# Kernel tuning notes

Hardware: AMD Instinct MI355X
Metric: run time of the kernel (lower is better)

## Reference

```python
import jax, jax.numpy as jnp
import numpy as np

N_NODES = 100000
N_EDGES = 1600000
IN_DIM, HIDDEN, OUT = 256, 128, 64


def setup_inputs() -> dict:
    key = jax.random.key(0)
    k1, k2, k3, k4 = jax.random.split(key, 4)
    x = jax.random.normal(k1, (N_NODES, IN_DIM), dtype=jnp.float32)
    edge_index = jax.random.randint(k2, (2, N_EDGES), 0, N_NODES, dtype=jnp.int32)
    # glorot-ish init for the GCN linear layers
    W1 = jax.random.normal(k3, (IN_DIM, HIDDEN), dtype=jnp.float32) / np.sqrt(IN_DIM)
    b1 = jnp.zeros((HIDDEN,), dtype=jnp.float32)
    W2 = jax.random.normal(k4, (HIDDEN, OUT), dtype=jnp.float32) / np.sqrt(HIDDEN)
    b2 = jnp.zeros((OUT,), dtype=jnp.float32)
    return {"x": x, "edge_index": edge_index, "W1": W1, "b1": b1, "W2": W2, "b2": b2}


def gcn_layer(x, src, dst, W, b):
    """PyG GCNConv: add self-loops, symmetric deg^-1/2 normalization,
    linear transform, scatter-add aggregation, bias."""
    h = x @ W  # [N, F_out]
    # degree over self-looped graph: in-degree(dst counts) + 1 self loop
    deg = jax.ops.segment_sum(jnp.ones((src.shape[0],), h.dtype), dst,
                              num_segments=N_NODES) + 1.0
    dinv = jax.lax.rsqrt(deg)  # [N]
    coef = dinv[src] * dinv[dst]  # [E]
    agg = jax.ops.segment_sum(h[src] * coef[:, None], dst, num_segments=N_NODES)
    # self-loop contribution (norm = dinv[i]^2) without materializing loop edges
    agg = agg + h * (dinv * dinv)[:, None]
    return agg + b


def reference(x, edge_index, W1, b1, W2, b2):
    src, dst = edge_index[0], edge_index[1]
    h = jax.nn.relu(gcn_layer(x, src, dst, W1, b1))
    return jax.nn.relu(gcn_layer(h, src, dst, W2, b2))
```

## Files before the change

kernel.cpp:

```cpp
#include <hip/hip_runtime.h>

#define N_NODES 100000
#define N_EDGES 1600000
#define IN_DIM 256
#define HIDDEN 128
#define OUT_DIM 64
#define LDA 40

#define NBIN 391
#define NBLK3 256
#define CHUNK 6250
#define NMAT (NBIN * NBLK3)
#define NBLK_SCAN (NMAT / 256)
#define CAP 6144

typedef __bf16 bf16x8 __attribute__((ext_vector_type(8)));
typedef __bf16 bf16x4 __attribute__((ext_vector_type(4)));
typedef float f32x4 __attribute__((ext_vector_type(4)));

__launch_bounds__(256)
__global__ void k_hist(const int* __restrict__ dst, int* __restrict__ cnt2) {
    __shared__ int hist[NBIN];
    for (int i = threadIdx.x; i < NBIN; i += 256) hist[i] = 0;
    __syncthreads();
    int base = blockIdx.x * CHUNK;
    for (int i = threadIdx.x; i < CHUNK; i += 256)
        atomicAdd(&hist[dst[base + i] >> 8], 1);
    __syncthreads();
    for (int k = threadIdx.x; k < NBIN; k += 256)
        cnt2[k * NBLK3 + blockIdx.x] = hist[k];
}

__global__ void k_scan1(int* __restrict__ a, int* __restrict__ bsum) {
    __shared__ int tmp[256];
    int t = threadIdx.x;
    int i = blockIdx.x * 256 + t;
    int v = a[i];
    tmp[t] = v;
    __syncthreads();
    #pragma unroll
    for (int off = 1; off < 256; off <<= 1) {
        int p = (t >= off) ? tmp[t - off] : 0;
        __syncthreads();
        tmp[t] += p;
        __syncthreads();
    }
    a[i] = tmp[t] - v;
    if (t == 255) bsum[blockIdx.x] = tmp[255];
}

__global__ void k_scan2(int* __restrict__ bsum) {
    __shared__ int tmp[512];
    int t = threadIdx.x;
    int v = (t < NBLK_SCAN) ? bsum[t] : 0;
    tmp[t] = v;
    __syncthreads();
    #pragma unroll
    for (int off = 1; off < 512; off <<= 1) {
        int p = (t >= off) ? tmp[t - off] : 0;
        __syncthreads();
        tmp[t] += p;
        __syncthreads();
    }
    if (t < NBLK_SCAN) bsum[t] = tmp[t] - v;
}

__global__ void k_scan3(int* __restrict__ a, const int* __restrict__ bsum) {
    int i = blockIdx.x * 256 + threadIdx.x;
    a[i] += bsum[blockIdx.x];
}

__launch_bounds__(256)
__global__ void k_scatter_bins(const int* __restrict__ src, const int* __restrict__ dst,
                               const int* __restrict__ off2,
                               unsigned int* __restrict__ ebuf) {
    __shared__ int cursor[NBIN];
    for (int k = threadIdx.x; k < NBIN; k += 256)
        cursor[k] = off2[k * NBLK3 + blockIdx.x];
    __syncthreads();
    int base = blockIdx.x * CHUNK;
    for (int i = threadIdx.x; i < CHUNK; i += 256) {
        int s = src[base + i], d = dst[base + i];
        int pos = atomicAdd(&cursor[d >> 8], 1);
        ebuf[pos] = ((unsigned)s << 8) | (unsigned)(d & 255);
    }
}

__launch_bounds__(256)
__global__ void k_fine(const unsigned int* __restrict__ ebuf, const int* __restrict__ off2,
                       int* __restrict__ esrc, int* __restrict__ rowstart,
                       float* __restrict__ dinv) {
    __shared__ int hist[256];
    __shared__ int tmp[256];
    __shared__ int nodeoff[256];
    __shared__ int cursor[256];
    __shared__ unsigned int ed[CAP];
    __shared__ int sOut[CAP];

    const int k = blockIdx.x;
    const int t = threadIdx.x;
    const int e0 = off2[k * NBLK3];
    const int e1 = (k + 1 < NBIN) ? off2[(k + 1) * NBLK3] : N_EDGES;
    int m = e1 - e0;
    if (m > CAP) m = CAP;

    hist[t] = 0;
    __syncthreads();
    for (int i = t; i < m; i += 256) {
        unsigned v = ebuf[e0 + i];
        ed[i] = v;
        atomicAdd(&hist[v & 255], 1);
    }
    __syncthreads();

    int v = hist[t];
    tmp[t] = v;
    __syncthreads();
    #pragma unroll
    for (int off = 1; off < 256; off <<= 1) {
        int p = (t >= off) ? tmp[t - off] : 0;
        __syncthreads();
        tmp[t] += p;
        __syncthreads();
    }
    nodeoff[t] = tmp[t] - v;
    cursor[t] = tmp[t] - v;
    __syncthreads();

    for (int i = t; i < m; i += 256) {
        unsigned e = ed[i];
        int pos = atomicAdd(&cursor[e & 255], 1);
        sOut[pos] = (int)(e >> 8);
    }
    __syncthreads();

    for (int i = t; i < m; i += 256) esrc[e0 + i] = sOut[i];

    int n = k * 256 + t;
    if (n < N_NODES) {
        rowstart[n] = e0 + nodeoff[t];
        dinv[n] = rsqrtf((float)hist[t] + 1.0f);
    }
    if (k == 0 && t == 0) rowstart[N_NODES] = N_EDGES;
}

__launch_bounds__(256, 2)
__global__ void k_gemm1(const float* __restrict__ X, const float* __restrict__ W1,
                        __bf16* __restrict__ H) {
    __shared__ __attribute__((aligned(16))) __bf16 As[128 * LDA];
    __shared__ __attribute__((aligned(16))) __bf16 Bs[128 * LDA];

    const int t = threadIdx.x;
    const int wave = t >> 6;
    const int lane = t & 63;
    const int wr = wave >> 1, wc = wave & 1;
    const int lm = lane & 15;
    const int q = lane >> 4;
    const int row0 = blockIdx.x * 128;

    f32x4 acc[4][4] = {};

    for (int k0 = 0; k0 < IN_DIM; k0 += 32) {
        #pragma unroll
        for (int p = 0; p < 4; ++p) {
            int r = p * 32 + (t >> 3);
            int kk = (t & 7) * 4;
            int g = row0 + r;
            float4 v = make_float4(0.f, 0.f, 0.f, 0.f);
            if (g < N_NODES) v = *(const float4*)&X[g * IN_DIM + k0 + kk];
            __bf16* dp = &As[r * LDA + kk];
            dp[0] = (__bf16)v.x; dp[1] = (__bf16)v.y;
            dp[2] = (__bf16)v.z; dp[3] = (__bf16)v.w;
        }
        #pragma unroll
        for (int p = 0; p < 4; ++p) {
            int idx = p * 256 + t;
            int kk = idx >> 5;
            int c = (idx & 31) * 4;
            float4 v = *(const float4*)&W1[(k0 + kk) * HIDDEN + c];
            Bs[(c + 0) * LDA + kk] = (__bf16)v.x;
            Bs[(c + 1) * LDA + kk] = (__bf16)v.y;
            Bs[(c + 2) * LDA + kk] = (__bf16)v.z;
            Bs[(c + 3) * LDA + kk] = (__bf16)v.w;
        }
        __syncthreads();

        bf16x8 af[4], bfr[4];
        #pragma unroll
        for (int mi = 0; mi < 4; ++mi)
            af[mi] = *(const bf16x8*)&As[(wr * 64 + mi * 16 + lm) * LDA + q * 8];
        #pragma unroll
        for (int ni = 0; ni < 4; ++ni)
            bfr[ni] = *(const bf16x8*)&Bs[(wc * 64 + ni * 16 + lm) * LDA + q * 8];
        #pragma unroll
        for (int mi = 0; mi < 4; ++mi)
            #pragma unroll
            for (int ni = 0; ni < 4; ++ni)
                acc[mi][ni] = __builtin_amdgcn_mfma_f32_16x16x32_bf16(
                    af[mi], bfr[ni], acc[mi][ni], 0, 0, 0);
        __syncthreads();
    }

    #pragma unroll
    for (int mi = 0; mi < 4; ++mi) {
        #pragma unroll
        for (int r = 0; r < 4; ++r) {
            int grow = row0 + wr * 64 + mi * 16 + q * 4 + r;
            if (grow < N_NODES) {
                #pragma unroll
                for (int ni = 0; ni < 4; ++ni) {
                    int col = wc * 64 + ni * 16 + lm;
                    H[grow * HIDDEN + col] = (__bf16)acc[mi][ni][r];
                }
            }
        }
    }
}

__launch_bounds__(256)
__global__ void k_gather1(const int* __restrict__ rowstart, const int* __restrict__ esrc,
                          const float* __restrict__ dinv,
                          const __bf16* __restrict__ H, const float* __restrict__ b1,
                          __bf16* __restrict__ AGG) {
    int n = blockIdx.x * 16 + (threadIdx.x >> 4);
    if (n >= N_NODES) return;
    int j = (threadIdx.x & 15) * 8;

    float dn = dinv[n];
    float s = dn * dn;
    bf16x8 h = *(const bf16x8*)&H[n * HIDDEN + j];
    float acc[8];
    #pragma unroll
    for (int i = 0; i < 8; ++i) acc[i] = (float)h[i] * s;

    int p0 = rowstart[n], p1 = rowstart[n + 1];
    int p = p0;
    for (; p + 3 < p1; p += 4) {
        int s0 = esrc[p + 0], s1 = esrc[p + 1], s2 = esrc[p + 2], s3 = esrc[p + 3];
        float c0 = dinv[s0] * dn, c1 = dinv[s1] * dn;
        float c2 = dinv[s2] * dn, c3 = dinv[s3] * dn;
        bf16x8 v0 = *(const bf16x8*)&H[s0 * HIDDEN + j];
        bf16x8 v1 = *(const bf16x8*)&H[s1 * HIDDEN + j];
        bf16x8 v2 = *(const bf16x8*)&H[s2 * HIDDEN + j];
        bf16x8 v3 = *(const bf16x8*)&H[s3 * HIDDEN + j];
        #pragma unroll
        for (int i = 0; i < 8; ++i) acc[i] = fmaf((float)v0[i], c0, acc[i]);
        #pragma unroll
        for (int i = 0; i < 8; ++i) acc[i] = fmaf((float)v1[i], c1, acc[i]);
        #pragma unroll
        for (int i = 0; i < 8; ++i) acc[i] = fmaf((float)v2[i], c2, acc[i]);
        #pragma unroll
        for (int i = 0; i < 8; ++i) acc[i] = fmaf((float)v3[i], c3, acc[i]);
    }
    for (; p < p1; ++p) {
        int sidx = esrc[p];
        float c = dinv[sidx] * dn;
        bf16x8 v = *(const bf16x8*)&H[sidx * HIDDEN + j];
        #pragma unroll
        for (int i = 0; i < 8; ++i) acc[i] = fmaf((float)v[i], c, acc[i]);
    }

    float4 bb0 = *(const float4*)&b1[j];
    float4 bb1 = *(const float4*)&b1[j + 4];
    bf16x8 o;
    o[0] = (__bf16)fmaxf(acc[0] + bb0.x, 0.f);
    o[1] = (__bf16)fmaxf(acc[1] + bb0.y, 0.f);
    o[2] = (__bf16)fmaxf(acc[2] + bb0.z, 0.f);
    o[3] = (__bf16)fmaxf(acc[3] + bb0.w, 0.f);
    o[4] = (__bf16)fmaxf(acc[4] + bb1.x, 0.f);
    o[5] = (__bf16)fmaxf(acc[5] + bb1.y, 0.f);
    o[6] = (__bf16)fmaxf(acc[6] + bb1.z, 0.f);
    o[7] = (__bf16)fmaxf(acc[7] + bb1.w, 0.f);
    *(bf16x8*)&AGG[n * HIDDEN + j] = o;
}

__launch_bounds__(256, 2)
__global__ void k_gemm2(const __bf16* __restrict__ AGG, const float* __restrict__ W2,
                        __bf16* __restrict__ H2) {
    __shared__ __attribute__((aligned(16))) __bf16 As[128 * LDA];
    __shared__ __attribute__((aligned(16))) __bf16 Bs[64 * LDA];

    const int t = threadIdx.x;
    const int wave = t >> 6;
    const int lane = t & 63;
    const int lm = lane & 15;
    const int q = lane >> 4;
    const int row0 = blockIdx.x * 128;

    f32x4 acc[2][4] = {};

    for (int k0 = 0; k0 < HIDDEN; k0 += 32) {
        #pragma unroll
        for (int p = 0; p < 2; ++p) {
            int idx = p * 256 + t;
            int r = idx >> 2;
            int seg = (idx & 3) * 8;
            int g = row0 + r;
            uint4 v = make_uint4(0u, 0u, 0u, 0u);
            if (g < N_NODES) v = *(const uint4*)&AGG[g * HIDDEN + k0 + seg];
            *(uint4*)&As[r * LDA + seg] = v;
        }
        #pragma unroll
        for (int p = 0; p < 2; ++p) {
            int idx = p * 256 + t;
            int kk = idx >> 4;
            int c = (idx & 15) * 4;
            float4 v = *(const float4*)&W2[(k0 + kk) * OUT_DIM + c];
            Bs[(c + 0) * LDA + kk] = (__bf16)v.x;
            Bs[(c + 1) * LDA + kk] = (__bf16)v.y;
            Bs[(c + 2) * LDA + kk] = (__bf16)v.z;
            Bs[(c + 3) * LDA + kk] = (__bf16)v.w;
        }
        __syncthreads();

        bf16x8 af[2], bfr[4];
        #pragma unroll
        for (int mi = 0; mi < 2; ++mi)
            af[mi] = *(const bf16x8*)&As[(wave * 32 + mi * 16 + lm) * LDA + q * 8];
        #pragma unroll
        for (int ni = 0; ni < 4; ++ni)
            bfr[ni] = *(const bf16x8*)&Bs[(ni * 16 + lm) * LDA + q * 8];
        #pragma unroll
        for (int mi = 0; mi < 2; ++mi)
            #pragma unroll
            for (int ni = 0; ni < 4; ++ni)
                acc[mi][ni] = __builtin_amdgcn_mfma_f32_16x16x32_bf16(
                    af[mi], bfr[ni], acc[mi][ni], 0, 0, 0);
        __syncthreads();
    }

    #pragma unroll
    for (int mi = 0; mi < 2; ++mi) {
        #pragma unroll
        for (int r = 0; r < 4; ++r) {
            int grow = row0 + wave * 32 + mi * 16 + q * 4 + r;
            if (grow < N_NODES) {
                #pragma unroll
                for (int ni = 0; ni < 4; ++ni) {
                    int col = ni * 16 + lm;
                    H2[grow * OUT_DIM + col] = (__bf16)acc[mi][ni][r];
                }
            }
        }
    }
}

__launch_bounds__(256)
__global__ void k_gather2(const int* __restrict__ rowstart, const int* __restrict__ esrc,
                          const float* __restrict__ dinv,
                          const __bf16* __restrict__ H2, const float* __restrict__ b2,
                          float* __restrict__ OUT) {
    int n = blockIdx.x * 32 + (threadIdx.x >> 3);
    if (n >= N_NODES) return;
    int j = (threadIdx.x & 7) * 8;

    float dn = dinv[n];
    float s = dn * dn;
    bf16x8 h = *(const bf16x8*)&H2[n * OUT_DIM + j];
    float acc[8];
    #pragma unroll
    for (int i = 0; i < 8; ++i) acc[i] = (float)h[i] * s;

    int p0 = rowstart[n], p1 = rowstart[n + 1];
    int p = p0;
    for (; p + 3 < p1; p += 4) {
        int s0 = esrc[p + 0], s1 = esrc[p + 1], s2 = esrc[p + 2], s3 = esrc[p + 3];
        float c0 = dinv[s0] * dn, c1 = dinv[s1] * dn;
        float c2 = dinv[s2] * dn, c3 = dinv[s3] * dn;
        bf16x8 v0 = *(const bf16x8*)&H2[s0 * OUT_DIM + j];
        bf16x8 v1 = *(const bf16x8*)&H2[s1 * OUT_DIM + j];
        bf16x8 v2 = *(const bf16x8*)&H2[s2 * OUT_DIM + j];
        bf16x8 v3 = *(const bf16x8*)&H2[s3 * OUT_DIM + j];
        #pragma unroll
        for (int i = 0; i < 8; ++i) acc[i] = fmaf((float)v0[i], c0, acc[i]);
        #pragma unroll
        for (int i = 0; i < 8; ++i) acc[i] = fmaf((float)v1[i], c1, acc[i]);
        #pragma unroll
        for (int i = 0; i < 8; ++i) acc[i] = fmaf((float)v2[i], c2, acc[i]);
        #pragma unroll
        for (int i = 0; i < 8; ++i) acc[i] = fmaf((float)v3[i], c3, acc[i]);
    }
    for (; p < p1; ++p) {
        int sidx = esrc[p];
        float c = dinv[sidx] * dn;
        bf16x8 v = *(const bf16x8*)&H2[sidx * OUT_DIM + j];
        #pragma unroll
        for (int i = 0; i < 8; ++i) acc[i] = fmaf((float)v[i], c, acc[i]);
    }

    float4 bb0 = *(const float4*)&b2[j];
    float4 bb1 = *(const float4*)&b2[j + 4];
    float4 o0, o1;
    o0.x = fmaxf(acc[0] + bb0.x, 0.f);
    o0.y = fmaxf(acc[1] + bb0.y, 0.f);
    o0.z = fmaxf(acc[2] + bb0.z, 0.f);
    o0.w = fmaxf(acc[3] + bb0.w, 0.f);
    o1.x = fmaxf(acc[4] + bb1.x, 0.f);
    o1.y = fmaxf(acc[5] + bb1.y, 0.f);
    o1.z = fmaxf(acc[6] + bb1.z, 0.f);
    o1.w = fmaxf(acc[7] + bb1.w, 0.f);
    *(float4*)&OUT[n * OUT_DIM + j] = o0;
    *(float4*)&OUT[n * OUT_DIM + j + 4] = o1;
}

extern "C" void kernel_launch(void* const* d_in, const int* in_sizes, int n_in,
                              void* d_out, int out_size, void* d_ws, size_t ws_size,
                              hipStream_t stream) {
    const float* x  = (const float*)d_in[0];
    const int* ei   = (const int*)d_in[1];
    const float* W1 = (const float*)d_in[2];
    const float* b1 = (const float*)d_in[3];
    const float* W2 = (const float*)d_in[4];
    const float* b2 = (const float*)d_in[5];
    float* out = (float*)d_out;

    const int* src = ei;
    const int* dst = ei + N_EDGES;

    char* ws = (char*)d_ws;
    int*          cnt2     = (int*)         (ws + 0x000000);
    int*          bsum     = (int*)         (ws + 0x080000);
    int*          rowstart = (int*)         (ws + 0x090000);
    float*        dinv     = (float*)       (ws + 0x100000);
    unsigned int* ebuf     = (unsigned int*)(ws + 0x180000);
    int*          esrc     = (int*)         (ws + 0x800000);
    __bf16*       h1       = (__bf16*)      (ws + 0xE80000);
    __bf16*       agg1     = (__bf16*)      (ws + 0x2880000);
    __bf16*       h2       = (__bf16*)      (ws + 0x4280000);

    k_hist<<<NBLK3, 256, 0, stream>>>(dst, cnt2);
    k_scan1<<<NBLK_SCAN, 256, 0, stream>>>(cnt2, bsum);
    k_scan2<<<1, 512, 0, stream>>>(bsum);
    k_scan3<<<NBLK_SCAN, 256, 0, stream>>>(cnt2, bsum);
    k_scatter_bins<<<NBLK3, 256, 0, stream>>>(src, dst, cnt2, ebuf);
    k_fine<<<NBIN, 256, 0, stream>>>(ebuf, cnt2, esrc, rowstart, dinv);

    k_gemm1<<<(N_NODES + 127) / 128, 256, 0, stream>>>(x, W1, h1);
    k_gather1<<<(N_NODES + 15) / 16, 256, 0, stream>>>(rowstart, esrc, dinv, h1, b1, agg1);
    k_gemm2<<<(N_NODES + 127) / 128, 256, 0, stream>>>(agg1, W2, h2);
    k_gather2<<<(N_NODES + 31) / 32, 256, 0, stream>>>(rowstart, esrc, dinv, h2, b2, out);
}
```

Before: 349.0 us.

## Load A operands directly from global into registers and stage full weight matrix in LDS

```diff
diff --git a/kernel.cpp b/kernel.cpp
--- a/kernel.cpp
+++ b/kernel.cpp
@@ -5,7 +5,6 @@
 #define IN_DIM 256
 #define HIDDEN 128
 #define OUT_DIM 64
-#define LDA 40
 
 #define NBIN 391
 #define NBLK3 256
@@ -13,6 +12,9 @@
 #define NMAT (NBIN * NBLK3)
 #define NBLK_SCAN (NMAT / 256)
 #define CAP 6144
+
+#define LDK1 264
+#define LDK2 136
 
 typedef __bf16 bf16x8 __attribute__((ext_vector_type(8)));
 typedef __bf16 bf16x4 __attribute__((ext_vector_type(4)));
@@ -147,8 +149,7 @@
 __launch_bounds__(256, 2)
 __global__ void k_gemm1(const float* __restrict__ X, const float* __restrict__ W1,
                         __bf16* __restrict__ H) {
-    __shared__ __attribute__((aligned(16))) __bf16 As[128 * LDA];
-    __shared__ __attribute__((aligned(16))) __bf16 Bs[128 * LDA];
+    __shared__ __attribute__((aligned(16))) __bf16 Bs[HIDDEN * LDK1];
 
     const int t = threadIdx.x;
     const int wave = t >> 6;
@@ -156,62 +157,71 @@
     const int wr = wave >> 1, wc = wave & 1;
     const int lm = lane & 15;
     const int q = lane >> 4;
-    const int row0 = blockIdx.x * 128;
+    const int row0 = blockIdx.x * 128 + wr * 64;
+    const int colbase = wc * 64;
+
+    #pragma unroll
+    for (int it = 0; it < 16; ++it) {
+        int idx = it * 256 + t;
+        int k2 = idx >> 5;
+        int c = (idx & 31) * 4;
+        float4 v0 = *(const float4*)&W1[(2 * k2) * HIDDEN + c];
+        float4 v1 = *(const float4*)&W1[(2 * k2 + 1) * HIDDEN + c];
+        const float lo[4] = {v0.x, v0.y, v0.z, v0.w};
+        const float hi[4] = {v1.x, v1.y, v1.z, v1.w};
+        #pragma unroll
+        for (int i = 0; i < 4; ++i) {
+            __bf16 pair[2] = {(__bf16)lo[i], (__bf16)hi[i]};
+            *(unsigned int*)&Bs[(c + i) * LDK1 + 2 * k2] = *(unsigned int*)pair;
+        }
+    }
+    __syncthreads();
+
+    const float* xp[4];
+    #pragma unroll
+    for (int mi = 0; mi < 4; ++mi) {
+        int r = row0 + mi * 16 + lm;
+        if (r > N_NODES - 1) r = N_NODES - 1;
+        xp[mi] = &X[r * IN_DIM];
+    }
 
     f32x4 acc[4][4] = {};
 
-    for (int k0 = 0; k0 < IN_DIM; k0 += 32) {
-        #pragma unroll
-        for (int p = 0; p < 4; ++p) {
-            int r = p * 32 + (t >> 3);
-            int kk = (t & 7) * 4;
-            int g = row0 + r;
-            float4 v = make_float4(0.f, 0.f, 0.f, 0.f);
-            if (g < N_NODES) v = *(const float4*)&X[g * IN_DIM + k0 + kk];
-            __bf16* dp = &As[r * LDA + kk];
-            dp[0] = (__bf16)v.x; dp[1] = (__bf16)v.y;
-            dp[2] = (__bf16)v.z; dp[3] = (__bf16)v.w;
+    #pragma unroll
+    for (int ks = 0; ks < 8; ++ks) {
+        bf16x8 af[4];
+        #pragma unroll
+        for (int mi = 0; mi < 4; ++mi) {
+            float4 a0 = *(const float4*)&xp[mi][ks * 32 + q * 8];
+            float4 a1 = *(const float4*)&xp[mi][ks * 32 + q * 8 + 4];
+            bf16x8 f;
+            f[0] = (__bf16)a0.x; f[1] = (__bf16)a0.y;
+            f[2] = (__bf16)a0.z; f[3] = (__bf16)a0.w;
+            f[4] = (__bf16)a1.x; f[5] = (__bf16)a1.y;
+            f[6] = (__bf16)a1.z; f[7] = (__bf16)a1.w;
+            af[mi] = f;
         }
-        #pragma unroll
-        for (int p = 0; p < 4; ++p) {
-            int idx = p * 256 + t;
-            int kk = idx >> 5;
-            int c = (idx & 31) * 4;
-            float4 v = *(const float4*)&W1[(k0 + kk) * HIDDEN + c];
-            Bs[(c + 0) * LDA + kk] = (__bf16)v.x;
-            Bs[(c + 1) * LDA + kk] = (__bf16)v.y;
-            Bs[(c + 2) * LDA + kk] = (__bf16)v.z;
-            Bs[(c + 3) * LDA + kk] = (__bf16)v.w;
-        }
-        __syncthreads();
-
-        bf16x8 af[4], bfr[4];
-        #pragma unroll
-        for (int mi = 0; mi < 4; ++mi)
-            af[mi] = *(const bf16x8*)&As[(wr * 64 + mi * 16 + lm) * LDA + q * 8];
+        bf16x8 bfr[4];
         #pragma unroll
         for (int ni = 0; ni < 4; ++ni)
-            bfr[ni] = *(const bf16x8*)&Bs[(wc * 64 + ni * 16 + lm) * LDA + q * 8];
+            bfr[ni] = *(const bf16x8*)&Bs[(colbase + ni * 16 + lm) * LDK1 + ks * 32 + q * 8];
         #pragma unroll
         for (int mi = 0; mi < 4; ++mi)
             #pragma unroll
             for (int ni = 0; ni < 4; ++ni)
                 acc[mi][ni] = __builtin_amdgcn_mfma_f32_16x16x32_bf16(
                     af[mi], bfr[ni], acc[mi][ni], 0, 0, 0);
-        __syncthreads();
     }
 
     #pragma unroll
     for (int mi = 0; mi < 4; ++mi) {
         #pragma unroll
         for (int r = 0; r < 4; ++r) {
-            int grow = row0 + wr * 64 + mi * 16 + q * 4 + r;
+            int grow = row0 + mi * 16 + q * 4 + r;
             if (grow < N_NODES) {
                 #pragma unroll
-                for (int ni = 0; ni < 4; ++ni) {
-                    int col = wc * 64 + ni * 16 + lm;
-                    H[grow * HIDDEN + col] = (__bf16)acc[mi][ni][r];
-                }
+                for (int ni = 0; ni < 4; ++ni)
+                    H[grow * HIDDEN + colbase + ni * 16 + lm] = (__bf16)acc[mi][ni][r];
             }
         }
     }
@@ -277,69 +287,69 @@
 __launch_bounds__(256, 2)
 __global__ void k_gemm2(const __bf16* __restrict__ AGG, const float* __restrict__ W2,
                         __bf16* __restrict__ H2) {
-    __shared__ __attribute__((aligned(16))) __bf16 As[128 * LDA];
-    __shared__ __attribute__((aligned(16))) __bf16 Bs[64 * LDA];
+    __shared__ __attribute__((aligned(16))) __bf16 Bs[OUT_DIM * LDK2];
 
     const int t = threadIdx.x;
     const int wave = t >> 6;
     const int lane = t & 63;
     const int lm = lane & 15;
     const int q = lane >> 4;
-    const int row0 = blockIdx.x * 128;
-
-    f32x4 acc[2][4] = {};
-
-    for (int k0 = 0; k0 < HIDDEN; k0 += 32) {
-        #pragma unroll
-        for (int p = 0; p < 2; ++p) {
-            int idx = p * 256 + t;
-            int r = idx >> 2;
-            int seg = (idx & 3) * 8;
-            int g = row0 + r;
-            uint4 v = make_uint4(0u, 0u, 0u, 0u);
-            if (g < N_NODES) v = *(const uint4*)&AGG[g * HIDDEN + k0 + seg];
-            *(uint4*)&As[r * LDA + seg] = v;
+    const int row0 = blockIdx.x * 256 + wave * 64;
+
+    #pragma unroll
+    for (int it = 0; it < 4; ++it) {
+        int idx = it * 256 + t;
+        int k2 = idx >> 4;
+        int c = (idx & 15) * 4;
+        float4 v0 = *(const float4*)&W2[(2 * k2) * OUT_DIM + c];
+        float4 v1 = *(const float4*)&W2[(2 * k2 + 1) * OUT_DIM + c];
+        const float lo[4] = {v0.x, v0.y, v0.z, v0.w};
+        const float hi[4] = {v1.x, v1.y, v1.z, v1.w};
+        #pragma unroll
+        for (int i = 0; i < 4; ++i) {
+            __bf16 pair[2] = {(__bf16)lo[i], (__bf16)hi[i]};
+            *(unsigned int*)&Bs[(c + i) * LDK2 + 2 * k2] = *(unsigned int*)pair;
         }
-        #pragma unroll
-        for (int p = 0; p < 2; ++p) {
-            int idx = p * 256 + t;
-            int kk = idx >> 4;
-            int c = (idx & 15) * 4;
-            float4 v = *(const float4*)&W2[(k0 + kk) * OUT_DIM + c];
-            Bs[(c + 0) * LDA + kk] = (__bf16)v.x;
-            Bs[(c + 1) * LDA + kk] = (__bf16)v.y;
-            Bs[(c + 2) * LDA + kk] = (__bf16)v.z;
-            Bs[(c + 3) * LDA + kk] = (__bf16)v.w;
-        }
-        __syncthreads();
-
-        bf16x8 af[2], bfr[4];
-        #pragma unroll
-        for (int mi = 0; mi < 2; ++mi)
-            af[mi] = *(const bf16x8*)&As[(wave * 32 + mi * 16 + lm) * LDA + q * 8];
+    }
+    __syncthreads();
+
+    const __bf16* ap[4];
+    #pragma unroll
+    for (int mi = 0; mi < 4; ++mi) {
+        int r = row0 + mi * 16 + lm;
+        if (r > N_NODES - 1) r = N_NODES - 1;
+        ap[mi] = &AGG[r * HIDDEN];
+    }
+
+    f32x4 acc[4][4] = {};
+
+    #pragma unroll
+    for (int ks = 0; ks < 4; ++ks) {
+        bf16x8 af[4];
+        #pragma unroll
+        for (int mi = 0; mi < 4; ++mi)
+            af[mi] = *(const bf16x8*)&ap[mi][ks * 32 + q * 8];
+        bf16x8 bfr[4];
         #pragma unroll
         for (int ni = 0; ni < 4; ++ni)
-            bfr[ni] = *(const bf16x8*)&Bs[(ni * 16 + lm) * LDA + q * 8];
-        #pragma unroll
-        for (int mi = 0; mi < 2; ++mi)
+            bfr[ni] = *(const bf16x8*)&Bs[(ni * 16 + lm) * LDK2 + ks * 32 + q * 8];
+        #pragma unroll
+        for (int mi = 0; mi < 4; ++mi)
             #pragma unroll
             for (int ni = 0; ni < 4; ++ni)
                 acc[mi][ni] = __builtin_amdgcn_mfma_f32_16x16x32_bf16(
                     af[mi], bfr[ni], acc[mi][ni], 0, 0, 0);
-        __syncthreads();
-    }
-
-    #pragma unroll
-    for (int mi = 0; mi < 2; ++mi) {
+    }
+
+    #pragma unroll
+    for (int mi = 0; mi < 4; ++mi) {
         #pragma unroll
         for (int r = 0; r < 4; ++r) {
-            int grow = row0 + wave * 32 + mi * 16 + q * 4 + r;
+            int grow = row0 + mi * 16 + q * 4 + r;
             if (grow < N_NODES) {
                 #pragma unroll
-                for (int ni = 0; ni < 4; ++ni) {
-                    int col = ni * 16 + lm;
-                    H2[grow * OUT_DIM + col] = (__bf16)acc[mi][ni][r];
-                }
+                for (int ni = 0; ni < 4; ++ni)
+                    H2[grow * OUT_DIM + ni * 16 + lm] = (__bf16)acc[mi][ni][r];
             }
         }
     }
@@ -437,6 +447,6 @@
 
     k_gemm1<<<(N_NODES + 127) / 128, 256, 0, stream>>>(x, W1, h1);
     k_gather1<<<(N_NODES + 15) / 16, 256, 0, stream>>>(rowstart, esrc, dinv, h1, b1, agg1);
-    k_gemm2<<<(N_NODES + 127) / 128, 256, 0, stream>>>(agg1, W2, h2);
+    k_gemm2<<<(N_NODES + 255) / 256, 256, 0, stream>>>(agg1, W2, h2);
     k_gather2<<<(N_NODES + 31) / 32, 256, 0, stream>>>(rowstart, esrc, dinv, h2, b2, out);
 }
```

Measured after the change: 356.2 us. 2.1% more time.
